# Optimization experiments

Hardware: AMD Instinct MI355X
Metric: run time of the kernel (lower is better)

Reference implementation:

```python
import jax, jax.numpy as jnp
import numpy as np
import math

B, T, DIM = 4, 4096, 1024
HID = int(DIM * 1.5)  # 1536
K = 4                  # conv kernel size
S = 16                 # num_slots
D = 384                # slot_dim


def setup_inputs() -> dict:
    key = jax.random.key(0)
    ks = jax.random.split(key, 16)
    inp = {
        "x": jax.random.normal(ks[0], (B, T, DIM), jnp.float32),
        "input_w": jax.random.normal(ks[1], (2 * HID, DIM), jnp.float32) * DIM ** -0.5,
        "conv_w": jax.random.normal(ks[2], (HID, K), jnp.float32) * K ** -0.5,
        "conv_b": jnp.zeros((HID,), jnp.float32),
        "gates_w": jax.random.normal(ks[3], (2 * HID, HID), jnp.float32) * HID ** -0.5,
        "gates_b": jnp.zeros((2 * HID,), jnp.float32),
        "forget_base": jnp.linspace(-4.323, -9.0, HID).astype(jnp.float32),
        "output_w": jax.random.normal(ks[4], (DIM, HID), jnp.float32) * HID ** -0.5,
        "memory_slots": jax.random.normal(ks[5], (S, D), jnp.float32) * 0.02,
        "wq_w": jax.random.normal(ks[6], (D, D), jnp.float32) * 0.02,
        "wk_w": jax.random.normal(ks[7], (D, HID), jnp.float32) * 0.02,
        "wv_w": jax.random.normal(ks[8], (D, HID), jnp.float32) * 0.02,
        "wg_w": jax.random.normal(ks[9], (1, HID), jnp.float32) * 0.02,
        "rq_w": jax.random.normal(ks[10], (D, HID), jnp.float32) * 0.02,
        "rk_w": jax.random.normal(ks[11], (D, D), jnp.float32) * 0.02,
        "rv_w": jax.random.normal(ks[12], (HID, D), jnp.float32) * 0.02,
    }
    return inp


def _causal_dwconv(x, w, b):
    # x: [B,T,H], w: [H,K], b: [H]; torch Conv1d(padding=K-1) then [:, :T] == causal
    xp = jnp.pad(x, ((0, 0), (K - 1, 0), (0, 0)))
    taps = jnp.stack([xp[:, j:j + T, :] for j in range(K)], axis=-1)  # [B,T,H,K]
    return jnp.einsum('bthk,hk->bth', taps, w) + b


def _scan(alpha, x):
    # h_t = alpha_t * h_{t-1} + x_t, elementwise over channels; along axis 1 (time)
    def combine(c1, c2):
        a1, b1 = c1
        a2, b2 = c2
        return a1 * a2, a2 * b1 + b2
    return jax.lax.associative_scan(combine, (alpha, x), axis=1)[1]


def reference(x, input_w, conv_w, conv_b, gates_w, gates_b, forget_base, output_w,
              memory_slots, wq_w, wk_w, wv_w, wg_w, rq_w, rk_w, rv_w):
    L = T // S  # segment length
    proj = x @ input_w.T                       # [B,T,2H]
    gate, xh = proj[..., :HID], proj[..., HID:]
    xh = _causal_dwconv(xh, conv_w, conv_b)    # [B,T,H]
    g = xh @ gates_w.T + gates_b               # [B,T,2H]
    forget, inp = g[..., :HID], g[..., HID:]
    alpha = jnp.exp(-8.0 * jax.nn.softplus(forget_base) * jax.nn.sigmoid(forget))
    xh = jnp.sqrt(1.0 - alpha ** 2 + 1e-6) * jax.nn.sigmoid(inp) * xh
    h = _scan(alpha, xh)                       # [B,T,H]
    xh = gate * jax.nn.sigmoid(gate) * xh      # silu-gated

    # ---- write_memory(xh) ----
    xseg = xh.reshape(B, S, L, HID)
    q = memory_slots @ wq_w.T                  # [S,D]
    kmat = jnp.einsum('bslh,dh->bsld', xseg, wk_w)
    vmat = jnp.einsum('bslh,dh->bsld', xseg, wv_w)
    qk = jnp.einsum('sd,bsld->bsl', q, kmat) / math.sqrt(D)
    attn = jax.nn.softmax(qk, axis=-1)
    mem = jnp.einsum('bsl,bsld->bsd', attn, vmat)  # [B,S,D]

    # ---- read_memory(gelu(xh)*h, mem) ----
    xr = jax.nn.gelu(xh, approximate=False) * h    # [B,T,H]
    rq = xr @ rq_w.T                               # [B,T,D]
    rk = mem @ rk_w.T                              # [B,S,D]
    rv = mem @ rv_w.T                              # [B,S,H]
    qk2 = jnp.einsum('btd,bsd->bts', rq, rk) / math.sqrt(D)
    seg = jnp.arange(T) // L
    mask = seg[:, None] <= jnp.arange(S)[None, :]  # [T,S]
    qk2 = jnp.where(mask[None], qk2, -jnp.inf)
    attn2 = jax.nn.softmax(qk2, axis=-1)
    out = jnp.einsum('bts,bsh->bth', attn2, rv)
    out = jax.nn.sigmoid(xr @ wg_w.T) * out        # write_gate on xr
    return out @ output_w.T                        # [B,T,DIM]
```

## Files before the change

kernel.cpp:

```cpp
#include <hip/hip_runtime.h>
#include <math.h>

#define BB 4
#define TT 4096
#define DIMW 1024
#define HID 1536
#define HID2 3072
#define KC 4
#define SSEG 16
#define LSEG 256
#define DD 384
#define NCH 64
#define CHL 64
#define TH  ((size_t)TT*(size_t)HID)
#define RKVN (DD + HID)

typedef _Float16 h8 __attribute__((ext_vector_type(8)));
typedef float f4 __attribute__((ext_vector_type(4)));

#define RSCL 4.8828125e-4f

__device__ __forceinline__ void hsplit(float a, _Float16& h0, _Float16& h1)
{
    _Float16 t = (_Float16)a;
    float tf = (float)t;
    if (fabsf(tf) < 6.103515625e-05f) { t = (_Float16)0.f; tf = 0.f; }
    h0 = t;
    h1 = (_Float16)((a - tf) * 2048.0f);
}

__device__ __forceinline__ void gl_lds16(const _Float16* g, _Float16* l)
{
    __builtin_amdgcn_global_load_lds(
        (const __attribute__((address_space(1))) unsigned int*)g,
        (__attribute__((address_space(3))) unsigned int*)l,
        16, 0, 0);
}

__global__ __launch_bounds__(256) void split2t(const float* __restrict__ src,
                                               _Float16* __restrict__ dst,
                                               int R, int Kd, size_t ps)
{
    __shared__ float tile[64][65];
    const int tid = threadIdx.x;
    const int bx = blockIdx.x;
    const int by = blockIdx.y;
    {
        const int lr = tid >> 2;
        const int lc = (tid & 3) * 16;
        const float* s = src + (size_t)(by * 64 + lr) * Kd + bx * 64 + lc;
#pragma unroll
        for (int e = 0; e < 16; e++) tile[lr][lc + e] = s[e];
    }
    __syncthreads();
    const int c = tid >> 5;
    const int r0 = tid & 31;
#pragma unroll
    for (int rr = 0; rr < 2; rr++) {
        const int r = r0 + rr * 32;
        h8 h0v, h1v;
#pragma unroll
        for (int e = 0; e < 8; e++) {
            _Float16 a0, a1;
            hsplit(tile[r][c * 8 + e], a0, a1);
            h0v[e] = a0; h1v[e] = a1;
        }
        const size_t didx = ((size_t)(bx * 8 + c) * R + by * 64 + r) * 8;
        *(h8*)(dst + didx) = h0v;
        *(h8*)(dst + ps + didx) = h1v;
    }
}

__global__ __launch_bounds__(256) void ccat2_kernel(const float* __restrict__ s1, int n1,
                                                    const float* __restrict__ s2, int n2,
                                                    float* __restrict__ dst)
{
    int i = blockIdx.x * 256 + threadIdx.x;
    if (i < n1) dst[i] = s1[i];
    else if (i < n1 + n2) dst[i] = s2[i - n1];
}

template<int MODE, int TM, int TN>
__global__ __launch_bounds__(512, 4) void gemm_mfma(
    const _Float16* __restrict__ Ap, size_t aps,
    const _Float16* __restrict__ Wp, size_t wps,
    float* __restrict__ C0, float* __restrict__ C1,
    const float* __restrict__ X,
    _Float16* __restrict__ OP, size_t ops,
    int M, int Nout, int Kd)
{
    constexpr int WTM = TM / 2, WTN = TN / 4;
    constexpr int MI = WTM / 16, NI = WTN / 16;
    static_assert(MI * NI <= 16, "DUAL only");
    constexpr int API = TM / 16;
    constexpr int BPI = TN / 16;
    constexpr int ATOT = 2 * API;
    constexpr int NISS = ATOT + 2 * BPI;
    static_assert(NISS % 8 == 0, "issue count must divide 8 waves");
    constexpr int PW = NISS / 8;

    __shared__ _Float16 Als[2][2][TM * 32];
    __shared__ _Float16 Bls[2][2][TN * 32];

    const int tid = threadIdx.x;
    const int lane = tid & 63;
    const int wv = tid >> 6;
    const int wr = wv >> 2, wc = wv & 3;
    const int lr = lane & 15, lg = lane >> 4;

    int bx = blockIdx.x, by = blockIdx.y;
    {
        const int gx = gridDim.x;
        const int nwg = gx * gridDim.y;
        if ((nwg & 7) == 0) {
            int wg = by * gx + bx;
            wg = (wg & 7) * (nwg >> 3) + (wg >> 3);
            bx = wg % gx; by = wg / gx;
        }
    }
    const int m0 = bx * TM, n0 = by * TN;

    f4 acc1[MI][NI], acc2[MI][NI];
#pragma unroll
    for (int i = 0; i < MI; i++)
#pragma unroll
        for (int j = 0; j < NI; j++) {
            acc1[i][j] = (f4){0.f, 0.f, 0.f, 0.f};
            acc2[i][j] = (f4){0.f, 0.f, 0.f, 0.f};
        }

    auto stage = [&](int kq0, int buf) {
#pragma unroll
        for (int j = 0; j < PW; j++) {
            const int i = j * 8 + wv;
            if (i < ATOT) {
                const int pl = i / API, s = i - pl * API;
                const int kc = (s * 64) / TM, r0 = (s * 64) % TM;
                gl_lds16(Ap + pl * aps + ((size_t)(kq0 + kc) * M + m0 + r0) * 8 + lane * 8,
                         &Als[buf][pl][(kc * TM + r0) * 8]);
            } else {
                const int jj = i - ATOT;
                const int pl = jj / BPI, s = jj - pl * BPI;
                const int kc = (s * 64) / TN, r0 = (s * 64) % TN;
                gl_lds16(Wp + pl * wps + ((size_t)(kq0 + kc) * Nout + n0 + r0) * 8 + lane * 8,
                         &Bls[buf][pl][(kc * TN + r0) * 8]);
            }
        }
    };

    stage(0, 0);
    __syncthreads();

    const int NS = Kd / 32;
    for (int t = 0; t < NS; t++) {
        const int buf = t & 1;
        if (t + 1 < NS) stage((t + 1) * 4, buf ^ 1);

        h8 af0[MI], af1[MI];
#pragma unroll
        for (int mi = 0; mi < MI; mi++) {
            const int arow = wr * WTM + mi * 16 + lr;
            af0[mi] = *(const h8*)&Als[buf][0][(lg * TM + arow) * 8];
            af1[mi] = *(const h8*)&Als[buf][1][(lg * TM + arow) * 8];
        }
#pragma unroll
        for (int ni = 0; ni < NI; ni++) {
            const int brow = wc * WTN + ni * 16 + lr;
            h8 b0 = *(const h8*)&Bls[buf][0][(lg * TN + brow) * 8];
            h8 b1 = *(const h8*)&Bls[buf][1][(lg * TN + brow) * 8];
#pragma unroll
            for (int mi = 0; mi < MI; mi++) {
                acc1[mi][ni] = __builtin_amdgcn_mfma_f32_16x16x32_f16(af0[mi], b0, acc1[mi][ni], 0, 0, 0);
                acc2[mi][ni] = __builtin_amdgcn_mfma_f32_16x16x32_f16(af1[mi], b0, acc2[mi][ni], 0, 0, 0);
                acc2[mi][ni] = __builtin_amdgcn_mfma_f32_16x16x32_f16(af0[mi], b1, acc2[mi][ni], 0, 0, 0);
            }
        }
        __syncthreads();
    }

#pragma unroll
    for (int mi = 0; mi < MI; mi++) {
#pragma unroll
        for (int ni = 0; ni < NI; ni++) {
#pragma unroll
            for (int r = 0; r < 4; r++) {
                const float v = acc1[mi][ni][r] + acc2[mi][ni][r] * RSCL;
                const int m = m0 + wr * WTM + mi * 16 + lg * 4 + r;
                const int n = n0 + wc * WTN + ni * 16 + lr;
                if constexpr (MODE == 1) {
                    if (n < HID) C0[(size_t)m * HID + n] = v;
                    else         C1[(size_t)m * HID + (n - HID)] = v;
                } else if constexpr (MODE == 2) {
                    float g = v;
                    float fv = (g / (1.0f + expf(-g))) * X[(size_t)m * Nout + n];
                    C0[(size_t)m * Nout + n] = fv;
                    _Float16 a0, a1;
                    hsplit(fv, a0, a1);
                    const size_t didx = ((size_t)(n >> 3) * M + m) * 8 + (n & 7);
                    OP[didx] = a0;
                    OP[ops + didx] = a1;
                } else {
                    C0[(size_t)m * Nout + n] = v;
                }
            }
        }
    }
}

template<int TM, int TN>
__global__ __launch_bounds__(256) void gemm32(const float* __restrict__ A,
                                              const float* __restrict__ W,
                                              float* __restrict__ C0,
                                              int M, int Nout, int Kd)
{
    constexpr int GM = TM / 64;
    constexpr int GN = TN / 64;
    constexpr int AF4 = TM * 4;
    constexpr int WF4 = TN * 4;
    constexpr int ALOOP = (AF4 + 255) / 256;
    constexpr int WLOOP = (WF4 + 255) / 256;

    __shared__ float As[16][TM];
    __shared__ float Bs[16][TN];

    const int tid = threadIdx.x;
    const int m0 = blockIdx.x * TM;
    const int n0 = blockIdx.y * TN;
    const int tx = tid & 15, ty = tid >> 4;

    float acc[GM * 4][GN * 4];
#pragma unroll
    for (int i = 0; i < GM * 4; i++)
#pragma unroll
        for (int j = 0; j < GN * 4; j++) acc[i][j] = 0.0f;

    float4 aReg[ALOOP], wReg[WLOOP];

    auto issueLoads = [&](int k0) {
#pragma unroll
        for (int u = 0; u < ALOOP; u++) {
            const int idx = tid + u * 256;
            float4 v = make_float4(0.f, 0.f, 0.f, 0.f);
            if (idx < AF4) {
                const int row = idx >> 2, kq = (idx & 3) * 4;
                const long ar = (long)(m0 + row);
                if (ar < M) v = *(const float4*)(A + ar * (long)Kd + (k0 + kq));
            }
            aReg[u] = v;
        }
#pragma unroll
        for (int u = 0; u < WLOOP; u++) {
            const int idx = tid + u * 256;
            float4 v = make_float4(0.f, 0.f, 0.f, 0.f);
            if (idx < WF4) {
                const int row = idx >> 2, kq = (idx & 3) * 4;
                const long wr = (long)(n0 + row);
                if (wr < Nout) v = *(const float4*)(W + wr * (long)Kd + (k0 + kq));
            }
            wReg[u] = v;
        }
    };
    auto writeLDS = [&]() {
#pragma unroll
        for (int u = 0; u < ALOOP; u++) {
            const int idx = tid + u * 256;
            if (idx < AF4) {
                const int row = idx >> 2, kq = (idx & 3) * 4;
                As[kq + 0][row] = aReg[u].x;
                As[kq + 1][row] = aReg[u].y;
                As[kq + 2][row] = aReg[u].z;
                As[kq + 3][row] = aReg[u].w;
            }
        }
#pragma unroll
        for (int u = 0; u < WLOOP; u++) {
            const int idx = tid + u * 256;
            if (idx < WF4) {
                const int row = idx >> 2, kq = (idx & 3) * 4;
                Bs[kq + 0][row] = wReg[u].x;
                Bs[kq + 1][row] = wReg[u].y;
                Bs[kq + 2][row] = wReg[u].z;
                Bs[kq + 3][row] = wReg[u].w;
            }
        }
    };

    issueLoads(0);
    writeLDS();
    __syncthreads();

    const int NT = Kd / 16;
    for (int t = 0; t < NT; t++) {
        if (t + 1 < NT) issueLoads((t + 1) * 16);
#pragma unroll
        for (int k = 0; k < 16; k++) {
            float a[GM * 4], b[GN * 4];
#pragma unroll
            for (int g = 0; g < GM; g++) {
                const float4 t4 = *(const float4*)&As[k][g * 64 + ty * 4];
                a[g * 4 + 0] = t4.x; a[g * 4 + 1] = t4.y;
                a[g * 4 + 2] = t4.z; a[g * 4 + 3] = t4.w;
            }
#pragma unroll
            for (int g = 0; g < GN; g++) {
                const float4 t4 = *(const float4*)&Bs[k][g * 64 + tx * 4];
                b[g * 4 + 0] = t4.x; b[g * 4 + 1] = t4.y;
                b[g * 4 + 2] = t4.z; b[g * 4 + 3] = t4.w;
            }
#pragma unroll
            for (int i = 0; i < GM * 4; i++)
#pragma unroll
                for (int j = 0; j < GN * 4; j++) acc[i][j] += a[i] * b[j];
        }
        __syncthreads();
        if (t + 1 < NT) {
            writeLDS();
            __syncthreads();
        }
    }

#pragma unroll
    for (int i = 0; i < GM * 4; i++) {
        const int m = m0 + (i >> 2) * 64 + ty * 4 + (i & 3);
        if (m >= M) continue;
#pragma unroll
        for (int j = 0; j < GN * 4; j++) {
            const int n = n0 + (j >> 2) * 64 + tx * 4 + (j & 3);
            if (n >= Nout) continue;
            C0[(long)m * Nout + n] = acc[i][j];
        }
    }
}

__global__ __launch_bounds__(256) void spb_kernel(const float* __restrict__ fb,
                                                  double* __restrict__ spb)
{
    int h = blockIdx.x * 256 + threadIdx.x;
    if (h < HID) {
        double xv = (double)fb[h];
        spb[h] = log1p(exp(xv));
    }
}

__global__ __launch_bounds__(256) void conv_kernel(const float* __restrict__ xin,
                                                   const float* __restrict__ cw,
                                                   const float* __restrict__ cb,
                                                   float* __restrict__ outp,
                                                   _Float16* __restrict__ outP,
                                                   size_t ps)
{
    size_t i = (size_t)blockIdx.x * 256 + threadIdx.x;
    if (i >= TH) return;
    int h = (int)(i % HID);
    int t = (int)(i / HID);
    float acc = cb[h];
#pragma unroll
    for (int j = 0; j < KC; j++) {
        int tt = t - (KC - 1) + j;
        if (tt >= 0) acc = fmaf(cw[h * KC + j], xin[(size_t)tt * HID + h], acc);
    }
    outp[i] = acc;
    _Float16 a0, a1;
    hsplit(acc, a0, a1);
    const size_t didx = ((size_t)(h >> 3) * TT + t) * 8 + (h & 7);
    outP[didx] = a0;
    outP[ps + didx] = a1;
}

__global__ __launch_bounds__(256) void alpha_xh2_kernel(float* __restrict__ fg,
                                                        float* __restrict__ ip,
                                                        const float* __restrict__ xh1,
                                                        const double* __restrict__ spb,
                                                        const float* __restrict__ gb)
{
    size_t i = (size_t)blockIdx.x * 256 + threadIdx.x;
    if (i >= TH) return;
    int h = (int)(i % HID);
    double f  = (double)fg[i] + (double)gb[h];
    float g2 = ip[i] + gb[HID + h];
    double sigf = 1.0 / (1.0 + exp(-f));
    float alpha = (float)exp(-8.0 * spb[h] * sigf);
    float s2 = sqrtf(1.0f - alpha * alpha + 1e-6f);
    float sigi = 1.0f / (1.0f + expf(-g2));
    fg[i] = alpha;
    ip[i] = s2 * sigi * xh1[i];
}

__global__ __launch_bounds__(256) void scan1_kernel(const float* __restrict__ alpha,
                                                    const float* __restrict__ xh2,
                                                    double* __restrict__ cA,
                                                    double* __restrict__ cB)
{
    int idx = blockIdx.x * 256 + threadIdx.x;
    if (idx >= NCH * HID) return;
    int h = idx % HID;
    int c = idx / HID;
    size_t base = (size_t)c * CHL * HID + h;
    double aP = 1.0, bV = 0.0;
    for (int i = 0; i < CHL; i++) {
        double a  = (double)alpha[base + (size_t)i * HID];
        double xv = (double)xh2 [base + (size_t)i * HID];
        bV = a * bV + xv;
        aP *= a;
    }
    size_t o = (size_t)c * HID + h;
    cA[o] = aP;
    cB[o] = bV;
}

__global__ __launch_bounds__(256) void scan2_kernel(const double* __restrict__ cA,
                                                    const double* __restrict__ cB,
                                                    double* __restrict__ cH0)
{
    int h = blockIdx.x * 256 + threadIdx.x;
    if (h >= HID) return;
    double carry = 0.0;
    for (int c = 0; c < NCH; c++) {
        size_t o = (size_t)c * HID + h;
        cH0[o] = carry;
        carry = cA[o] * carry + cB[o];
    }
}

__global__ __launch_bounds__(256) void scan3gelu_kernel(const float* __restrict__ alpha,
                                                        const float* __restrict__ xh2,
                                                        const double* __restrict__ cH0,
                                                        float* __restrict__ xh3,
                                                        _Float16* __restrict__ outP,
                                                        size_t ps)
{
    int idx = blockIdx.x * 256 + threadIdx.x;
    if (idx >= NCH * HID) return;
    int h = idx % HID;
    int c = idx / HID;
    size_t base = (size_t)c * CHL * HID + h;
    double hv = cH0[(size_t)c * HID + h];
    for (int i = 0; i < CHL; i++) {
        size_t off = base + (size_t)i * HID;
        double a  = (double)alpha[off];
        double xv = (double)xh2 [off];
        hv = a * hv + xv;
        float x3 = xh3[off];
        float ge = 0.5f * x3 * (1.0f + erff(x3 * 0.70710678f));
        float fv = ge * (float)hv;
        xh3[off] = fv;
        _Float16 a0, a1;
        hsplit(fv, a0, a1);
        const int t = c * CHL + i;
        const size_t didx = ((size_t)(h >> 3) * TT + t) * 8 + (h & 7);
        outP[didx] = a0;
        outP[ps + didx] = a1;
    }
}

__global__ __launch_bounds__(256) void attn1_kernel(const float* __restrict__ kv,
                                                    const float* __restrict__ qbuf,
                                                    float* __restrict__ mem)
{
    const int s = blockIdx.x;
    const int l = threadIdx.x;
    const size_t row = (size_t)s * LSEG + l;
    const float* kr = kv + row * (2 * DD);
    const float* qs = qbuf + (size_t)s * DD;
    double acc = 0.0;
    for (int d = 0; d < DD; d++) acc += (double)qs[d] * (double)kr[d];
    double qk = acc / sqrt((double)DD);
    __shared__ double r1[256];
    __shared__ double sw[256];
    r1[l] = qk; __syncthreads();
    for (int off = 128; off > 0; off >>= 1) {
        if (l < off) r1[l] = fmax(r1[l], r1[l + off]);
        __syncthreads();
    }
    double m = r1[0]; __syncthreads();
    double e = exp(qk - m);
    r1[l] = e; __syncthreads();
    for (int off = 128; off > 0; off >>= 1) {
        if (l < off) r1[l] += r1[l + off];
        __syncthreads();
    }
    double denom = r1[0];
    sw[l] = e / denom; __syncthreads();
    const size_t vbase = (size_t)s * LSEG * (2 * DD) + DD;
    for (int d = l; d < DD; d += 256) {
        double a2 = 0.0;
        for (int ll = 0; ll < LSEG; ll++)
            a2 += sw[ll] * (double)kv[vbase + (size_t)ll * (2 * DD) + d];
        mem[(size_t)s * DD + d] = (float)a2;
    }
}

__global__ __launch_bounds__(256) void attn2_kernel(const float* __restrict__ rq,
                                                    const float* __restrict__ rkv,
                                                    const float* __restrict__ xr,
                                                    const float* __restrict__ wg,
                                                    _Float16* __restrict__ outP,
                                                    size_t ps)
{
    const int t = blockIdx.x;
    const int sigma = t >> 8;
    const int tid = threadIdx.x;
    __shared__ double sqk[16];
    __shared__ double red[256];
    __shared__ double sw[16];
    __shared__ double sgate;

    const float* rqn = rq + (size_t)t * DD;
    {
        int s = tid >> 4, j = tid & 15;
        const float* rks = rkv + (size_t)s * RKVN;
        double part = 0.0;
        for (int d = j; d < DD; d += 16) part += (double)rqn[d] * (double)rks[d];
#pragma unroll
        for (int off = 8; off > 0; off >>= 1) part += __shfl_down(part, off, 16);
        if (j == 0) sqk[s] = part;
    }
    double gp = 0.0;
    const float* xrn = xr + (size_t)t * HID;
    for (int hh = tid; hh < HID; hh += 256) gp += (double)xrn[hh] * (double)wg[hh];
    red[tid] = gp; __syncthreads();
    for (int off = 128; off > 0; off >>= 1) {
        if (tid < off) red[tid] += red[tid + off];
        __syncthreads();
    }
    if (tid == 0) {
        const double inv = 1.0 / sqrt((double)DD);
        double m = -1e300;
        for (int ss = sigma; ss < 16; ss++) {
            double v = sqk[ss] * inv;
            sqk[ss] = v;
            if (v > m) m = v;
        }
        double sum = 0.0;
        for (int ss = sigma; ss < 16; ss++) {
            double e = exp(sqk[ss] - m);
            sw[ss] = e;
            sum += e;
        }
        double isum = 1.0 / sum;
        for (int ss = 0; ss < sigma; ss++) sw[ss] = 0.0;
        for (int ss = sigma; ss < 16; ss++) sw[ss] *= isum;
        sgate = 1.0 / (1.0 + exp(-red[0]));
    }
    __syncthreads();
    const double gte = sgate;
    for (int c = tid; c < HID / 8; c += 256) {
        double accv[8] = {0, 0, 0, 0, 0, 0, 0, 0};
        for (int ss = sigma; ss < 16; ss++) {
            const float* rvp = rkv + (size_t)ss * RKVN + DD + c * 8;
            double w = sw[ss];
#pragma unroll
            for (int e = 0; e < 8; e++) accv[e] += w * (double)rvp[e];
        }
        h8 h0v, h1v;
#pragma unroll
        for (int e = 0; e < 8; e++) {
            _Float16 a0, a1;
            hsplit((float)(gte * accv[e]), a0, a1);
            h0v[e] = a0; h1v[e] = a1;
        }
        const size_t didx = ((size_t)c * TT + t) * 8;
        *(h8*)(outP + didx) = h0v;
        *(h8*)(outP + ps + didx) = h1v;
    }
}

extern "C" void kernel_launch(void* const* d_in, const int* in_sizes, int n_in,
                              void* d_out, int out_size, void* d_ws, size_t ws_size,
                              hipStream_t stream)
{
    const float* x            = (const float*)d_in[0];
    const float* input_w      = (const float*)d_in[1];
    const float* conv_w       = (const float*)d_in[2];
    const float* conv_b       = (const float*)d_in[3];
    const float* gates_w      = (const float*)d_in[4];
    const float* gates_b      = (const float*)d_in[5];
    const float* forget_base  = (const float*)d_in[6];
    const float* output_w     = (const float*)d_in[7];
    const float* memory_slots = (const float*)d_in[8];
    const float* wq_w         = (const float*)d_in[9];
    const float* wk_w         = (const float*)d_in[10];
    const float* wv_w         = (const float*)d_in[11];
    const float* wg_w         = (const float*)d_in[12];
    const float* rq_w         = (const float*)d_in[13];
    const float* rk_w         = (const float*)d_in[14];
    const float* rv_w         = (const float*)d_in[15];
    float* out = (float*)d_out;

    double* spb  = (double*)d_ws;
    double* cA   = spb + HID;
    double* cB   = cA + (size_t)NCH * HID;
    double* cH0  = cB + (size_t)NCH * HID;
    float* slotA = (float*)(cH0 + (size_t)NCH * HID);
    float* slotB = slotA + TH;
    float* slotC = slotB + TH;
    float* qbuf   = slotC + TH;
    float* membuf = qbuf + (size_t)SSEG * DD;
    float* rkvw   = membuf + (size_t)SSEG * DD;
    float* rkvbuf = rkvw + (size_t)RKVN * DD;
    float* kvbuf  = rkvbuf + (size_t)SSEG * RKVN;

    _Float16* base_h = (_Float16*)(kvbuf + (size_t)TT * 2 * DD);
    const size_t iwN  = (size_t)HID * DIMW;
    const size_t gwN  = (size_t)HID2 * HID;
    const size_t kvN  = (size_t)(2 * DD) * HID;
    const size_t rqN  = (size_t)DD * HID;
    const size_t owN  = (size_t)DIMW * HID;
    const size_t xbN  = (size_t)TT * DIMW;
    _Float16* iwlo = base_h;
    _Float16* iwhi = iwlo + 2 * iwN;
    _Float16* gwp  = iwhi + 2 * iwN;
    _Float16* wkvp = gwp  + 2 * gwN;
    _Float16* rqwp = wkvp + 2 * kvN;
    _Float16* owp  = rqwp + 2 * rqN;
    _Float16* xbP  = owp  + 2 * owN;
    _Float16* P1   = xbP  + 2 * xbN;

    dim3 blk(256);
    dim3 blk512(512);
    const int ewBlocks = (int)(TH / 256);

    spb_kernel<<<(HID + 255) / 256, blk, 0, stream>>>(forget_base, spb);
    ccat2_kernel<<<(2 * DD * HID + 255) / 256, blk, 0, stream>>>(
        wk_w, DD * HID, wv_w, DD * HID, slotA);
    ccat2_kernel<<<(RKVN * DD + 255) / 256, blk, 0, stream>>>(
        rk_w, DD * DD, rv_w, HID * DD, rkvw);
    split2t<<<dim3(DIMW / 64, HID / 64), blk, 0, stream>>>(input_w, iwlo, HID, DIMW, iwN);
    split2t<<<dim3(DIMW / 64, HID / 64), blk, 0, stream>>>(input_w + (size_t)HID * DIMW,
                                                           iwhi, HID, DIMW, iwN);
    split2t<<<dim3(HID / 64, HID2 / 64), blk, 0, stream>>>(gates_w, gwp, HID2, HID, gwN);
    split2t<<<dim3(HID / 64, (2 * DD) / 64), blk, 0, stream>>>(slotA, wkvp, 2 * DD, HID, kvN);
    split2t<<<dim3(HID / 64, DD / 64), blk, 0, stream>>>(rq_w, rqwp, DD, HID, rqN);
    split2t<<<dim3(HID / 64, DIMW / 64), blk, 0, stream>>>(output_w, owp, DIMW, HID, owN);
    gemm32<64, 64><<<dim3(1, DD / 64), blk, 0, stream>>>(
        memory_slots, wq_w, qbuf, SSEG, DD, DD);

    for (int b = 0; b < BB; b++) {
        const float* xb   = x   + (size_t)b * TT * DIMW;
        float*       outb = out + (size_t)b * TT * DIMW;

        split2t<<<dim3(DIMW / 64, TT / 64), blk, 0, stream>>>(xb, xbP, TT, DIMW, xbN);
        gemm_mfma<0, 128, 128><<<dim3(TT / 128, HID / 128), blk512, 0, stream>>>(
            xbP, xbN, iwhi, iwN, slotB, (float*)nullptr, (const float*)nullptr,
            (_Float16*)nullptr, 0, TT, HID, DIMW);
        conv_kernel<<<ewBlocks, blk, 0, stream>>>(slotB, conv_w, conv_b, slotC, P1, TH);
        gemm_mfma<1, 128, 128><<<dim3(TT / 128, HID2 / 128), blk512, 0, stream>>>(
            P1, TH, gwp, gwN, slotA, slotB, (const float*)nullptr,
            (_Float16*)nullptr, 0, TT, HID2, HID);
        alpha_xh2_kernel<<<ewBlocks, blk, 0, stream>>>(slotA, slotB, slotC, spb, gates_b);
        scan1_kernel<<<(NCH * HID) / 256, blk, 0, stream>>>(slotA, slotB, cA, cB);
        scan2_kernel<<<(HID + 255) / 256, blk, 0, stream>>>(cA, cB, cH0);
        gemm_mfma<2, 128, 128><<<dim3(TT / 128, HID / 128), blk512, 0, stream>>>(
            xbP, xbN, iwlo, iwN, slotC, (float*)nullptr, slotB, P1, TH, TT, HID, DIMW);
        gemm_mfma<0, 128, 128><<<dim3(TT / 128, (2 * DD) / 128), blk512, 0, stream>>>(
            P1, TH, wkvp, kvN, kvbuf, (float*)nullptr, (const float*)nullptr,
            (_Float16*)nullptr, 0, TT, 2 * DD, HID);
        attn1_kernel<<<SSEG, blk, 0, stream>>>(kvbuf, qbuf, membuf);
        gemm32<64, 64><<<dim3(1, (RKVN + 63) / 64), blk, 0, stream>>>(
            membuf, rkvw, rkvbuf, SSEG, RKVN, DD);
        scan3gelu_kernel<<<(NCH * HID) / 256, blk, 0, stream>>>(
            slotA, slotB, cH0, slotC, P1, TH);
        gemm_mfma<0, 64, 128><<<dim3(TT / 64, DD / 128), blk512, 0, stream>>>(
            P1, TH, rqwp, rqN, slotB, (float*)nullptr, (const float*)nullptr,
            (_Float16*)nullptr, 0, TT, DD, HID);
        attn2_kernel<<<TT, blk, 0, stream>>>(slotB, rkvbuf, slotC, wg_w, P1, TH);
        gemm_mfma<0, 128, 128><<<dim3(TT / 128, DIMW / 128), blk512, 0, stream>>>(
            P1, TH, owp, owN, outb, (float*)nullptr, (const float*)nullptr,
            (_Float16*)nullptr, 0, TT, DIMW, HID);
    }
}
```

Before: 2.474 ms.

## Fuse alpha computation into chunk scan; add 2x2 XCD tile swizzle; retile KV GEMM

Merges the elementwise alpha/xh2 kernel into the first chunked-scan pass, so alpha and gated input are computed and consumed in one sweep. This saves a full extra read of the gate tensors per batch. The fused kernel runs with far fewer threads (64x1536) than the old elementwise launch, which could lower latency hiding for the heavy double-precision exp. It also changes the GEMM workgroup remap to group 2x2 tiles per XCD for better L2 locality, and shrinks the KV projection GEMM tile to 64 rows to launch more workgroups.

```diff
diff --git a/kernel.cpp b/kernel.cpp
--- a/kernel.cpp
+++ b/kernel.cpp
@@ -110,9 +110,18 @@
 
     int bx = blockIdx.x, by = blockIdx.y;
     {
-        const int gx = gridDim.x;
-        const int nwg = gx * gridDim.y;
-        if ((nwg & 7) == 0) {
+        const int gx = gridDim.x, gy = gridDim.y;
+        const int nwg = gx * gy;
+        if (((gx & 1) | (gy & 1)) == 0 && (nwg & 31) == 0) {
+            int wg = by * gx + bx;
+            const int xcd = wg & 7;
+            const int t = wg >> 3;
+            const int S = xcd * (nwg >> 5) + (t >> 2);
+            const int w = t & 3;
+            const int sgx = gx >> 1;
+            bx = (S % sgx) * 2 + (w & 1);
+            by = (S / sgx) * 2 + (w >> 1);
+        } else if ((nwg & 7) == 0) {
             int wg = by * gx + bx;
             wg = (wg & 7) * (nwg >> 3) + (wg >> 3);
             bx = wg % gx; by = wg / gx;
@@ -367,41 +376,37 @@
     outP[ps + didx] = a1;
 }
 
-__global__ __launch_bounds__(256) void alpha_xh2_kernel(float* __restrict__ fg,
-                                                        float* __restrict__ ip,
-                                                        const float* __restrict__ xh1,
-                                                        const double* __restrict__ spb,
-                                                        const float* __restrict__ gb)
-{
-    size_t i = (size_t)blockIdx.x * 256 + threadIdx.x;
-    if (i >= TH) return;
-    int h = (int)(i % HID);
-    double f  = (double)fg[i] + (double)gb[h];
-    float g2 = ip[i] + gb[HID + h];
-    double sigf = 1.0 / (1.0 + exp(-f));
-    float alpha = (float)exp(-8.0 * spb[h] * sigf);
-    float s2 = sqrtf(1.0f - alpha * alpha + 1e-6f);
-    float sigi = 1.0f / (1.0f + expf(-g2));
-    fg[i] = alpha;
-    ip[i] = s2 * sigi * xh1[i];
-}
-
-__global__ __launch_bounds__(256) void scan1_kernel(const float* __restrict__ alpha,
-                                                    const float* __restrict__ xh2,
-                                                    double* __restrict__ cA,
-                                                    double* __restrict__ cB)
+__global__ __launch_bounds__(256) void alphascan1_kernel(float* __restrict__ fg,
+                                                         float* __restrict__ ip,
+                                                         const float* __restrict__ xh1,
+                                                         const double* __restrict__ spb,
+                                                         const float* __restrict__ gb,
+                                                         double* __restrict__ cA,
+                                                         double* __restrict__ cB)
 {
     int idx = blockIdx.x * 256 + threadIdx.x;
     if (idx >= NCH * HID) return;
     int h = idx % HID;
     int c = idx / HID;
+    const double spbh = spb[h];
+    const float gbf = gb[h];
+    const float gbi = gb[HID + h];
     size_t base = (size_t)c * CHL * HID + h;
     double aP = 1.0, bV = 0.0;
     for (int i = 0; i < CHL; i++) {
-        double a  = (double)alpha[base + (size_t)i * HID];
-        double xv = (double)xh2 [base + (size_t)i * HID];
-        bV = a * bV + xv;
-        aP *= a;
+        size_t off = base + (size_t)i * HID;
+        double f = (double)fg[off] + (double)gbf;
+        float g2 = ip[off] + gbi;
+        double sigf = 1.0 / (1.0 + exp(-f));
+        double alpha = exp(-8.0 * spbh * sigf);
+        float af = (float)alpha;
+        float s2 = sqrtf(1.0f - af * af + 1e-6f);
+        float sigi = 1.0f / (1.0f + expf(-g2));
+        float x2 = s2 * sigi * xh1[off];
+        fg[off] = af;
+        ip[off] = x2;
+        bV = (double)af * bV + (double)x2;
+        aP *= (double)af;
     }
     size_t o = (size_t)c * HID + h;
     cA[o] = aP;
@@ -647,12 +652,12 @@
         gemm_mfma<1, 128, 128><<<dim3(TT / 128, HID2 / 128), blk512, 0, stream>>>(
             P1, TH, gwp, gwN, slotA, slotB, (const float*)nullptr,
             (_Float16*)nullptr, 0, TT, HID2, HID);
-        alpha_xh2_kernel<<<ewBlocks, blk, 0, stream>>>(slotA, slotB, slotC, spb, gates_b);
-        scan1_kernel<<<(NCH * HID) / 256, blk, 0, stream>>>(slotA, slotB, cA, cB);
+        alphascan1_kernel<<<(NCH * HID) / 256, blk, 0, stream>>>(
+            slotA, slotB, slotC, spb, gates_b, cA, cB);
         scan2_kernel<<<(HID + 255) / 256, blk, 0, stream>>>(cA, cB, cH0);
         gemm_mfma<2, 128, 128><<<dim3(TT / 128, HID / 128), blk512, 0, stream>>>(
             xbP, xbN, iwlo, iwN, slotC, (float*)nullptr, slotB, P1, TH, TT, HID, DIMW);
-        gemm_mfma<0, 128, 128><<<dim3(TT / 128, (2 * DD) / 128), blk512, 0, stream>>>(
+        gemm_mfma<0, 64, 128><<<dim3(TT / 64, (2 * DD) / 128), blk512, 0, stream>>>(
             P1, TH, wkvp, kvN, kvbuf, (float*)nullptr, (const float*)nullptr,
             (_Float16*)nullptr, 0, TT, 2 * DD, HID);
         attn1_kernel<<<SSEG, blk, 0, stream>>>(kvbuf, qbuf, membuf);
```

After: 2.415 ms. 2.4% less time.
